# Kernel optimization log

Measured on AMD Instinct MI355X. Metric: run time of the kernel, lower is better.

## Reference

```python
import jax, jax.numpy as jnp
import numpy as np

N_STEPS = 20      # max(n_steps_al, n_steps_kc)
ALPHA   = 0.9     # membrane decay exp(-dt/tau_m)
V_TH    = 1.0     # spiking threshold
G_SOMA  = 0.3     # dendrite->axon coupling conductance (2-compartment KC)
APL_GAIN = 1.0    # graded APL gain
I_SCALE = 0.5     # graded ORN drive scale
BETA    = 10.0    # surrogate-gradient sharpness ('soft' sigmoid)

@jax.custom_vjp
def spike(x):
    return (x > 0).astype(x.dtype)

def _spike_fwd(x):
    return spike(x), x

def _spike_bwd(x, g):
    s = jax.nn.sigmoid(BETA * x)
    return (g * BETA * s * (1.0 - s),)

spike.defvjp(_spike_fwd, _spike_bwd)


def _sparse_w(key, shape, density):
    k1, k2 = jax.random.split(key)
    mask = jax.random.bernoulli(k1, density, shape)
    w = jax.random.uniform(k2, shape)
    return (mask * w).astype(jnp.float32)


def setup_inputs() -> dict:
    key = jax.random.key(0)
    ks = jax.random.split(key, 10)
    batch, n_or, n_orn, n_ln, n_pn, n_kc, n_odors = 4096, 21, 42, 56, 42, 2000, 34
    or_input = jax.random.uniform(ks[0], (batch, n_or), dtype=jnp.float32)
    or_gains = jnp.ones((n_or,), jnp.float32)
    # fixed OR->ORN mapping: OR i drives left (2i) and right (2i+1) ORNs
    m = np.zeros((n_or, n_orn), np.float32)
    for i in range(n_or):
        m[i, 2 * i] = 1.0
        m[i, 2 * i + 1] = 1.0
    mapping = jnp.asarray(m)
    orn_to_pn = _sparse_w(ks[1], (n_orn, n_pn), 0.3)
    orn_to_ln = _sparse_w(ks[2], (n_orn, n_ln), 0.3)
    ln_to_pn = _sparse_w(ks[3], (n_ln, n_pn), 0.3)
    pn_to_kc = _sparse_w(ks[4], (n_pn, n_kc), 0.15)  # ~6 PN claws per KC
    kc_to_apl = jax.random.uniform(ks[5], (n_kc, 1), dtype=jnp.float32) * 0.01
    apl_to_kc = jax.random.uniform(ks[6], (1, n_kc), dtype=jnp.float32)
    dec_w = jax.random.normal(ks[7], (n_kc, n_odors), dtype=jnp.float32) * 0.02
    dec_b = jnp.zeros((n_odors,), jnp.float32)
    return {"or_input": or_input, "or_gains": or_gains, "mapping": mapping,
            "orn_to_pn": orn_to_pn, "orn_to_ln": orn_to_ln, "ln_to_pn": ln_to_pn,
            "pn_to_kc": pn_to_kc, "kc_to_apl": kc_to_apl, "apl_to_kc": apl_to_kc,
            "dec_w": dec_w, "dec_b": dec_b}


def reference(or_input, or_gains, mapping, orn_to_pn, orn_to_ln, ln_to_pn,
              pn_to_kc, kc_to_apl, apl_to_kc, dec_w, dec_b):
    B = or_input.shape[0]
    n_orn, n_pn = orn_to_pn.shape
    n_ln = orn_to_ln.shape[1]
    n_kc = pn_to_kc.shape[1]
    # OR transduction: graded, learnable per-OR gain
    orn_drive = (or_input * jax.nn.softplus(or_gains)) @ mapping  # [B, n_orn]

    z = lambda n: jnp.zeros((B, n), or_input.dtype)
    carry0 = (z(n_orn), z(n_ln), z(n_pn), z(n_kc), z(n_kc), z(1), z(n_kc))

    def step(carry, _):
        v_orn, v_ln, v_pn, v_d, v_a, apl, kc_cnt = carry
        # ORN LIF driven by graded OR current
        v_orn = ALPHA * v_orn + I_SCALE * orn_drive
        s_orn = spike(v_orn - V_TH)
        v_orn = v_orn * (1.0 - s_orn)
        # LN LIF (lateral inhibition interneurons)
        v_ln = ALPHA * v_ln + s_orn @ orn_to_ln
        s_ln = spike(v_ln - V_TH)
        v_ln = v_ln * (1.0 - s_ln)
        # PN LIF: ORN excitation, LN inhibition
        v_pn = ALPHA * v_pn + s_orn @ orn_to_pn - s_ln @ ln_to_pn
        s_pn = spike(v_pn - V_TH)
        v_pn = v_pn * (1.0 - s_pn)
        # KC 2-compartment: dendrite gets PN input and APL inhibition
        v_d = ALPHA * v_d + s_pn @ pn_to_kc - apl @ apl_to_kc
        v_a = ALPHA * v_a + G_SOMA * (v_d - v_a)
        s_kc = spike(v_a - V_TH)
        v_a = v_a * (1.0 - s_kc)
        # APL: graded (non-spiking) global inhibition from KC spikes
        apl = APL_GAIN * jax.nn.relu(s_kc @ kc_to_apl)
        return (v_orn, v_ln, v_pn, v_d, v_a, apl, kc_cnt + s_kc), None

    carry, _ = jax.lax.scan(step, carry0, None, length=N_STEPS)
    kc_count = carry[-1]
    kc_rates = kc_count / N_STEPS
    logits = kc_rates @ dec_w + dec_b  # [B, n_odors]
    return logits
```

## Files before the change

### kernel.cpp

```cpp
#include <hip/hip_runtime.h>

#define NSTEPS 20
#define ALPHA  0.9f
#define VTH    1.0f
#define GSOMA  0.3f
#define ISCALE 0.5f

#define NOR  21
#define NORN 42
#define NLN  56
#define NPN  42
#define NKC  2000
#define NOD  34

#define TPB  256
#define KPER 8

typedef float v2f __attribute__((ext_vector_type(2)));
typedef float v4f __attribute__((ext_vector_type(4)));

#define PK_ADD(d, a) asm("v_pk_add_f32 %0, %1, %0" : "+v"(d) : "v"(a))
#define PK_FMA(d, b, f) asm("v_pk_fma_f32 %0, %1, %2, %0" : "+v"(d) : "v"(b), "v"(f))

__global__ __launch_bounds__(64)
void phase1a(const float* __restrict__ or_input,
             const float* __restrict__ or_gains,
             const float* __restrict__ mapping,
             const float* __restrict__ orn_to_ln,
             ulonglong2* __restrict__ gAB,
             int batch)
{
    const int lane = threadIdx.x;
    const int row  = blockIdx.x;
    if (row >= batch) return;

    const int jl = lane < NLN ? lane : 0;
    float wOl[NORN];
#pragma unroll
    for (int o = 0; o < NORN; ++o) wOl[o] = orn_to_ln[o * NLN + jl];

    float spg = 0.f;
    if (lane < NOR) spg = log1pf(expf(or_gains[lane]));

    float drive = 0.f;
    {
        const float* x = or_input + (long)row * NOR;
        const int jo = lane < NORN ? lane : 0;
#pragma unroll
        for (int i = 0; i < NOR; ++i) {
            float g = __shfl(spg, i);
            drive += x[i] * g * mapping[i * NORN + jo];
        }
        drive *= ISCALE;
    }

    float v_orn = 0.f, v_ln = 0.f;
    ulonglong2* outm = gAB + (long)row * NSTEPS;

    for (int t = 0; t < NSTEPS; ++t) {
        bool so = false;
        if (lane < NORN) {
            v_orn = ALPHA * v_orn + drive;
            so = (v_orn - VTH) > 0.f;
            if (so) v_orn = 0.f;
        }
        const unsigned long long mOrn = __ballot(so);
        const unsigned int mo_lo = (unsigned int)mOrn;
        const unsigned int mo_hi = (unsigned int)(mOrn >> 32);

        float aln = 0.f;
#pragma unroll
        for (int o = 0; o < 32; ++o) aln += (float)((mo_lo >> o) & 1u) * wOl[o];
#pragma unroll
        for (int o = 32; o < NORN; ++o) aln += (float)((mo_hi >> (o - 32)) & 1u) * wOl[o];

        bool sl = false;
        if (lane < NLN) {
            v_ln = ALPHA * v_ln + aln;
            sl = (v_ln - VTH) > 0.f;
            if (sl) v_ln = 0.f;
        }
        const unsigned long long mLn = __ballot(sl);
        if (lane == 0) outm[t] = make_ulonglong2(mOrn, mLn);
    }
}

__global__ __launch_bounds__(64)
void phase1b(const float* __restrict__ orn_to_pn,
             const float* __restrict__ ln_to_pn,
             const ulonglong2* __restrict__ gAB,
             unsigned long long* __restrict__ gPN,
             int batch)
{
    const int lane = threadIdx.x;
    const int row  = blockIdx.x;
    if (row >= batch) return;

    const int jp = lane < NPN ? lane : 0;
    float wOp[NORN], wLp[NLN];
#pragma unroll
    for (int o = 0; o < NORN; ++o) wOp[o] = orn_to_pn[o * NPN + jp];
#pragma unroll
    for (int l = 0; l < NLN; ++l) wLp[l] = ln_to_pn[l * NPN + jp];

    const ulonglong2* inm = gAB + (long)row * NSTEPS;
    unsigned long long* outm = gPN + (long)row * NSTEPS;

    float v_pn = 0.f;
    ulonglong2 ab = inm[0];

    for (int t = 0; t < NSTEPS; ++t) {
        ulonglong2 abn;
        if (t < NSTEPS - 1) abn = inm[t + 1];

        const unsigned int mo_lo = (unsigned int)ab.x;
        const unsigned int mo_hi = (unsigned int)(ab.x >> 32);
        const unsigned int ml_lo = (unsigned int)ab.y;
        const unsigned int ml_hi = (unsigned int)(ab.y >> 32);

        float apn = 0.f;
#pragma unroll
        for (int o = 0; o < 32; ++o) apn += (float)((mo_lo >> o) & 1u) * wOp[o];
#pragma unroll
        for (int o = 32; o < NORN; ++o) apn += (float)((mo_hi >> (o - 32)) & 1u) * wOp[o];

        float h = 0.f;
#pragma unroll
        for (int l = 0; l < 32; ++l) h += (float)((ml_lo >> l) & 1u) * wLp[l];
#pragma unroll
        for (int l = 32; l < NLN; ++l) h += (float)((ml_hi >> (l - 32)) & 1u) * wLp[l];

        bool sp = false;
        if (lane < NPN) {
            v_pn = ALPHA * v_pn + apn - h;
            sp = (v_pn - VTH) > 0.f;
            if (sp) v_pn = 0.f;
        }
        const unsigned long long mPn = __ballot(sp);
        if (lane == 0) outm[t] = mPn;
        ab = abn;
    }
}

__global__ __launch_bounds__(TPB)
void phase2_pkc(const unsigned long long* __restrict__ g_masks,
                const float* __restrict__ pn_to_kc,
                const float* __restrict__ kc_to_apl,
                const float* __restrict__ apl_to_kc,
                const float* __restrict__ dec_w,
                const float* __restrict__ dec_b,
                float* __restrict__ out)
{
    __shared__ float sRed[2][4];
    __shared__ float sRed2[4 * NOD];

    const int tid  = threadIdx.x;
    const int lane = tid & 63;
    const int wid  = tid >> 6;
    const int b    = blockIdx.x;

    const int  kbase = tid * KPER;
    const bool act   = (kbase < NKC);
    v2f   vd2[4];
    float va[KPER], cnt[KPER], wa2k[KPER], wk2a[KPER];
#pragma unroll
    for (int k = 0; k < 4; ++k) vd2[k] = (v2f)(0.f);
#pragma unroll
    for (int j = 0; j < KPER; ++j) { va[j] = 0.f; cnt[j] = 0.f; }
    {
        const int idx = act ? kbase : 0;
        const float4* a4 = (const float4*)(apl_to_kc + idx);
        const float4* k4 = (const float4*)(kc_to_apl + idx);
        float4 a0 = a4[0], a1 = a4[1], k0 = k4[0], k1 = k4[1];
        const float g = act ? 1.f : 0.f;
        wa2k[0] = g * a0.x; wa2k[1] = g * a0.y; wa2k[2] = g * a0.z; wa2k[3] = g * a0.w;
        wa2k[4] = g * a1.x; wa2k[5] = g * a1.y; wa2k[6] = g * a1.z; wa2k[7] = g * a1.w;
        wk2a[0] = g * k0.x; wk2a[1] = g * k0.y; wk2a[2] = g * k0.z; wk2a[3] = g * k0.w;
        wk2a[4] = g * k1.x; wk2a[5] = g * k1.y; wk2a[6] = g * k1.z; wk2a[7] = g * k1.w;
    }
    if (tid < 8) sRed[tid >> 2][tid & 3] = 0.f;
    __syncthreads();

    const unsigned long long* gm = g_masks + (long)b * NSTEPS;
    unsigned long long mcur = gm[0];

    for (int t = 0; t < NSTEPS; ++t) {
        unsigned long long mnext;
        if (t < NSTEPS - 1) mnext = gm[t + 1];

        const float* rp = sRed[(t + 1) & 1];
        const float apl = fmaxf(rp[0] + rp[1] + rp[2] + rp[3], 0.f);

#pragma unroll
        for (int j = 0; j < KPER; ++j)
            vd2[j >> 1][j & 1] = ALPHA * vd2[j >> 1][j & 1] - apl * wa2k[j];

        unsigned long long m = mcur;
        while (m) {
            const int p0 = __builtin_ctzll(m); m &= m - 1;
            int p1 = p0; float f1 = 0.f;
            if (m) { p1 = __builtin_ctzll(m); m &= m - 1; f1 = 1.f; }
            if (act) {
                const v4f* w0 = (const v4f*)(pn_to_kc + (long)p0 * NKC + kbase);
                const v4f* w1 = (const v4f*)(pn_to_kc + (long)p1 * NKC + kbase);
                v4f A0 = w0[0], A1 = w0[1];
                v4f B0 = w1[0], B1 = w1[1];
                v2f f2; f2[0] = f1; f2[1] = f1;
                PK_ADD(vd2[0], A0.xy); PK_ADD(vd2[1], A0.zw);
                PK_ADD(vd2[2], A1.xy); PK_ADD(vd2[3], A1.zw);
                PK_FMA(vd2[0], B0.xy, f2); PK_FMA(vd2[1], B0.zw, f2);
                PK_FMA(vd2[2], B1.xy, f2); PK_FMA(vd2[3], B1.zw, f2);
            }
        }

        float aplp = 0.f;
#pragma unroll
        for (int j = 0; j < KPER; ++j) {
            va[j] = ALPHA * va[j] + GSOMA * (vd2[j >> 1][j & 1] - va[j]);
            const bool c = (va[j] - VTH) > 0.f;
            const float s = c ? 1.f : 0.f;
            va[j] = c ? 0.f : va[j];
            cnt[j] += s;
            aplp += s * wk2a[j];
        }
        for (int off = 32; off > 0; off >>= 1) aplp += __shfl_xor(aplp, off, 64);
        if (lane == 0) sRed[t & 1][wid] = aplp;
        __syncthreads();
        mcur = mnext;
    }

    float acc[NOD];
#pragma unroll
    for (int o = 0; o < NOD; ++o) acc[o] = 0.f;
    if (act) {
#pragma unroll
        for (int j = 0; j < KPER; ++j) {
            float r = cnt[j] / 20.0f;
            if (r != 0.f) {
                const float* wr = dec_w + (long)(kbase + j) * NOD;
#pragma unroll
                for (int o = 0; o < NOD; ++o) acc[o] += r * wr[o];
            }
        }
    }
#pragma unroll
    for (int o = 0; o < NOD; ++o) {
        float v = acc[o];
        for (int off = 32; off > 0; off >>= 1) v += __shfl_xor(v, off, 64);
        if (lane == 0) sRed2[wid * NOD + o] = v;
    }
    __syncthreads();
    if (tid < NOD) {
        float v = sRed2[tid] + sRed2[NOD + tid] + sRed2[2 * NOD + tid] +
                  sRed2[3 * NOD + tid] + dec_b[tid];
        out[(long)b * NOD + tid] = v;
    }
}

__global__ __launch_bounds__(TPB)
void snn_fused(const float* __restrict__ or_input, const float* __restrict__ or_gains,
               const float* __restrict__ mapping, const float* __restrict__ orn_to_pn,
               const float* __restrict__ orn_to_ln, const float* __restrict__ ln_to_pn,
               const float* __restrict__ pn_to_kc, const float* __restrict__ kc_to_apl,
               const float* __restrict__ apl_to_kc, const float* __restrict__ dec_w,
               const float* __restrict__ dec_b, float* __restrict__ out)
{
    __shared__ float sW_ol[NORN * NLN];
    __shared__ float sW_op[NORN * NPN];
    __shared__ float sW_lp[NLN * NPN];
    __shared__ float sDrive[NORN];
    __shared__ float sSpg[NOR];
    __shared__ float sOrn[NORN];
    __shared__ float sLn[NLN];
    __shared__ float sApl;
    __shared__ float sRed[4];
    __shared__ float sRed2[4 * NOD];
    __shared__ unsigned long long sMask;

    const int tid = threadIdx.x;
    const int b   = blockIdx.x;

    for (int i = tid; i < NORN * NLN; i += TPB) sW_ol[i] = orn_to_ln[i];
    for (int i = tid; i < NORN * NPN; i += TPB) sW_op[i] = orn_to_pn[i];
    for (int i = tid; i < NLN * NPN;  i += TPB) sW_lp[i] = ln_to_pn[i];
    if (tid < NOR) sSpg[tid] = log1pf(expf(or_gains[tid]));
    if (tid == 0)  sApl = 0.f;
    __syncthreads();

    if (tid < NORN) {
        const float* x = or_input + (long)b * NOR;
        float d = 0.f;
        for (int i = 0; i < NOR; ++i) d += x[i] * sSpg[i] * mapping[i * NORN + tid];
        sDrive[tid] = d * ISCALE;
    }

    const int  kbase = tid * KPER;
    const bool act   = (kbase < NKC);
    float vd[KPER], va[KPER], cnt[KPER], wa2k[KPER], wk2a[KPER];
#pragma unroll
    for (int j = 0; j < KPER; ++j) {
        vd[j] = 0.f; va[j] = 0.f; cnt[j] = 0.f;
        wa2k[j] = act ? apl_to_kc[kbase + j] : 0.f;
        wk2a[j] = act ? kc_to_apl[kbase + j] : 0.f;
    }
    float v_orn = 0.f, v_ln = 0.f, v_pn = 0.f, v_pn_exc = 0.f;
    __syncthreads();

    for (int t = 0; t < NSTEPS; ++t) {
        if (tid < NORN) {
            v_orn = ALPHA * v_orn + sDrive[tid];
            float s = (v_orn - VTH) > 0.f ? 1.f : 0.f;
            v_orn *= (1.f - s);
            sOrn[tid] = s;
        }
        __syncthreads();
        if (tid < NLN) {
            float a = 0.f;
            for (int o = 0; o < NORN; ++o) a += sOrn[o] * sW_ol[o * NLN + tid];
            v_ln = ALPHA * v_ln + a;
            float s = (v_ln - VTH) > 0.f ? 1.f : 0.f;
            v_ln *= (1.f - s);
            sLn[tid] = s;
        } else if (tid >= 64 && tid < 64 + NPN) {
            const int j = tid - 64;
            float a = 0.f;
            for (int o = 0; o < NORN; ++o) a += sOrn[o] * sW_op[o * NPN + j];
            v_pn_exc = a;
        }
        __syncthreads();
        if (tid >= 64 && tid < 64 + NPN) {
            const int j = tid - 64;
            float inh = 0.f;
            for (int l = 0; l < NLN; ++l) inh += sLn[l] * sW_lp[l * NPN + j];
            v_pn = ALPHA * v_pn + v_pn_exc - inh;
            bool s = (v_pn - VTH) > 0.f;
            if (s) v_pn = 0.f;
            unsigned long long bal = __ballot(s);
            if (tid == 64) sMask = bal;
        }
        __syncthreads();
        {
            const float apl = sApl;
#pragma unroll
            for (int j = 0; j < KPER; ++j) vd[j] = ALPHA * vd[j] - apl * wa2k[j];
            unsigned long long m = sMask;
            while (m) {
                const int p = __builtin_ctzll(m);
                m &= m - 1;
                if (act) {
                    const float4* w = (const float4*)(pn_to_kc + (long)p * NKC + kbase);
                    float4 w0 = w[0], w1 = w[1];
                    vd[0] += w0.x; vd[1] += w0.y; vd[2] += w0.z; vd[3] += w0.w;
                    vd[4] += w1.x; vd[5] += w1.y; vd[6] += w1.z; vd[7] += w1.w;
                }
            }
            float aplp = 0.f;
#pragma unroll
            for (int j = 0; j < KPER; ++j) {
                va[j] = ALPHA * va[j] + GSOMA * (vd[j] - va[j]);
                float s = (va[j] - VTH) > 0.f ? 1.f : 0.f;
                va[j] *= (1.f - s);
                cnt[j] += s;
                aplp += s * wk2a[j];
            }
            for (int off = 32; off > 0; off >>= 1) aplp += __shfl_xor(aplp, off, 64);
            if ((tid & 63) == 0) sRed[tid >> 6] = aplp;
        }
        __syncthreads();
        if (tid == 0) {
            float a = sRed[0] + sRed[1] + sRed[2] + sRed[3];
            sApl = fmaxf(a, 0.f);
        }
    }

    float acc[NOD];
#pragma unroll
    for (int o = 0; o < NOD; ++o) acc[o] = 0.f;
    if (act) {
#pragma unroll
        for (int j = 0; j < KPER; ++j) {
            float r = cnt[j] / 20.0f;
            if (r != 0.f) {
                const float* wr = dec_w + (long)(kbase + j) * NOD;
#pragma unroll
                for (int o = 0; o < NOD; ++o) acc[o] += r * wr[o];
            }
        }
    }
#pragma unroll
    for (int o = 0; o < NOD; ++o) {
        float v = acc[o];
        for (int off = 32; off > 0; off >>= 1) v += __shfl_xor(v, off, 64);
        if ((tid & 63) == 0) sRed2[(tid >> 6) * NOD + o] = v;
    }
    __syncthreads();
    if (tid < NOD) {
        float v = sRed2[tid] + sRed2[NOD + tid] + sRed2[2 * NOD + tid] +
                  sRed2[3 * NOD + tid] + dec_b[tid];
        out[(long)b * NOD + tid] = v;
    }
}

extern "C" void kernel_launch(void* const* d_in, const int* in_sizes, int n_in,
                              void* d_out, int out_size, void* d_ws, size_t ws_size,
                              hipStream_t stream) {
    (void)n_in; (void)out_size;
    const float* or_input  = (const float*)d_in[0];
    const float* or_gains  = (const float*)d_in[1];
    const float* mapping   = (const float*)d_in[2];
    const float* orn_to_pn = (const float*)d_in[3];
    const float* orn_to_ln = (const float*)d_in[4];
    const float* ln_to_pn  = (const float*)d_in[5];
    const float* pn_to_kc  = (const float*)d_in[6];
    const float* kc_to_apl = (const float*)d_in[7];
    const float* apl_to_kc = (const float*)d_in[8];
    const float* dec_w     = (const float*)d_in[9];
    const float* dec_b     = (const float*)d_in[10];
    float* out = (float*)d_out;

    const int batch = in_sizes[0] / NOR;
    const size_t needAB = (size_t)batch * NSTEPS * sizeof(ulonglong2);
    const size_t needPN = (size_t)batch * NSTEPS * sizeof(unsigned long long);

    if (ws_size >= needAB + needPN) {
        ulonglong2* gAB = (ulonglong2*)d_ws;
        unsigned long long* gPN = (unsigned long long*)((char*)d_ws + needAB);
        hipLaunchKernelGGL(phase1a, dim3(batch), dim3(64), 0, stream,
                           or_input, or_gains, mapping, orn_to_ln, gAB, batch);
        hipLaunchKernelGGL(phase1b, dim3(batch), dim3(64), 0, stream,
                           orn_to_pn, ln_to_pn, gAB, gPN, batch);
        hipLaunchKernelGGL(phase2_pkc, dim3(batch), dim3(TPB), 0, stream,
                           gPN, pn_to_kc, kc_to_apl, apl_to_kc, dec_w, dec_b, out);
    } else {
        hipLaunchKernelGGL(snn_fused, dim3(batch), dim3(TPB), 0, stream,
                           or_input, or_gains, mapping, orn_to_pn, orn_to_ln,
                           ln_to_pn, pn_to_kc, kc_to_apl, apl_to_kc, dec_w, dec_b, out);
    }
}
```

Measured before the change: 215.9 us.

## Run KC phase with a single wavefront per batch row to remove block barriers

```diff
diff --git a/kernel.cpp b/kernel.cpp
--- a/kernel.cpp
+++ b/kernel.cpp
@@ -15,12 +15,7 @@
 
 #define TPB  256
 #define KPER 8
-
-typedef float v2f __attribute__((ext_vector_type(2)));
-typedef float v4f __attribute__((ext_vector_type(4)));
-
-#define PK_ADD(d, a) asm("v_pk_add_f32 %0, %1, %0" : "+v"(d) : "v"(a))
-#define PK_FMA(d, b, f) asm("v_pk_fma_f32 %0, %1, %2, %0" : "+v"(d) : "v"(b), "v"(f))
+#define KPW  32
 
 __global__ __launch_bounds__(64)
 void phase1a(const float* __restrict__ or_input,
@@ -142,118 +137,136 @@
     }
 }
 
-__global__ __launch_bounds__(TPB)
-void phase2_pkc(const unsigned long long* __restrict__ g_masks,
-                const float* __restrict__ pn_to_kc,
-                const float* __restrict__ kc_to_apl,
-                const float* __restrict__ apl_to_kc,
-                const float* __restrict__ dec_w,
-                const float* __restrict__ dec_b,
-                float* __restrict__ out)
+__global__ __launch_bounds__(64)
+void phase2_w1(const unsigned long long* __restrict__ g_masks,
+               const float* __restrict__ pn_to_kc,
+               const float* __restrict__ kc_to_apl,
+               const float* __restrict__ apl_to_kc,
+               const float* __restrict__ dec_w,
+               const float* __restrict__ dec_b,
+               float* __restrict__ out)
 {
-    __shared__ float sRed[2][4];
-    __shared__ float sRed2[4 * NOD];
-
-    const int tid  = threadIdx.x;
-    const int lane = tid & 63;
-    const int wid  = tid >> 6;
-    const int b    = blockIdx.x;
-
-    const int  kbase = tid * KPER;
-    const bool act   = (kbase < NKC);
-    v2f   vd2[4];
-    float va[KPER], cnt[KPER], wa2k[KPER], wk2a[KPER];
-#pragma unroll
-    for (int k = 0; k < 4; ++k) vd2[k] = (v2f)(0.f);
-#pragma unroll
-    for (int j = 0; j < KPER; ++j) { va[j] = 0.f; cnt[j] = 0.f; }
-    {
-        const int idx = act ? kbase : 0;
-        const float4* a4 = (const float4*)(apl_to_kc + idx);
-        const float4* k4 = (const float4*)(kc_to_apl + idx);
-        float4 a0 = a4[0], a1 = a4[1], k0 = k4[0], k1 = k4[1];
-        const float g = act ? 1.f : 0.f;
-        wa2k[0] = g * a0.x; wa2k[1] = g * a0.y; wa2k[2] = g * a0.z; wa2k[3] = g * a0.w;
-        wa2k[4] = g * a1.x; wa2k[5] = g * a1.y; wa2k[6] = g * a1.z; wa2k[7] = g * a1.w;
-        wk2a[0] = g * k0.x; wk2a[1] = g * k0.y; wk2a[2] = g * k0.z; wk2a[3] = g * k0.w;
-        wk2a[4] = g * k1.x; wk2a[5] = g * k1.y; wk2a[6] = g * k1.z; wk2a[7] = g * k1.w;
-    }
-    if (tid < 8) sRed[tid >> 2][tid & 3] = 0.f;
-    __syncthreads();
+    const int lane  = threadIdx.x;
+    const int b     = blockIdx.x;
+    const int kbase = lane * KPW;
+
+    bool vk[4];
+#pragma unroll
+    for (int k = 0; k < 4; ++k) vk[k] = (kbase + k * 8) < NKC;
+
+    float vd[KPW], va[KPW], cnt[KPW], wa2k[KPW], wk2a[KPW];
+#pragma unroll
+    for (int j = 0; j < KPW; ++j) { vd[j] = 0.f; va[j] = 0.f; cnt[j] = 0.f; }
+
+#pragma unroll
+    for (int q = 0; q < 8; ++q) {
+        const int k   = q >> 1;
+        const int idx = vk[k] ? (kbase + q * 4) : 0;
+        const float g = vk[k] ? 1.f : 0.f;
+        float4 a = *(const float4*)(apl_to_kc + idx);
+        float4 c = *(const float4*)(kc_to_apl + idx);
+        wa2k[q * 4 + 0] = g * a.x; wa2k[q * 4 + 1] = g * a.y;
+        wa2k[q * 4 + 2] = g * a.z; wa2k[q * 4 + 3] = g * a.w;
+        wk2a[q * 4 + 0] = g * c.x; wk2a[q * 4 + 1] = g * c.y;
+        wk2a[q * 4 + 2] = g * c.z; wk2a[q * 4 + 3] = g * c.w;
+    }
 
     const unsigned long long* gm = g_masks + (long)b * NSTEPS;
     unsigned long long mcur = gm[0];
+    float apl = 0.f;
 
     for (int t = 0; t < NSTEPS; ++t) {
         unsigned long long mnext;
         if (t < NSTEPS - 1) mnext = gm[t + 1];
 
-        const float* rp = sRed[(t + 1) & 1];
-        const float apl = fmaxf(rp[0] + rp[1] + rp[2] + rp[3], 0.f);
-
-#pragma unroll
-        for (int j = 0; j < KPER; ++j)
-            vd2[j >> 1][j & 1] = ALPHA * vd2[j >> 1][j & 1] - apl * wa2k[j];
+#pragma unroll
+        for (int j = 0; j < KPW; ++j) vd[j] = ALPHA * vd[j] - apl * wa2k[j];
 
         unsigned long long m = mcur;
         while (m) {
             const int p0 = __builtin_ctzll(m); m &= m - 1;
             int p1 = p0; float f1 = 0.f;
             if (m) { p1 = __builtin_ctzll(m); m &= m - 1; f1 = 1.f; }
-            if (act) {
-                const v4f* w0 = (const v4f*)(pn_to_kc + (long)p0 * NKC + kbase);
-                const v4f* w1 = (const v4f*)(pn_to_kc + (long)p1 * NKC + kbase);
-                v4f A0 = w0[0], A1 = w0[1];
-                v4f B0 = w1[0], B1 = w1[1];
-                v2f f2; f2[0] = f1; f2[1] = f1;
-                PK_ADD(vd2[0], A0.xy); PK_ADD(vd2[1], A0.zw);
-                PK_ADD(vd2[2], A1.xy); PK_ADD(vd2[3], A1.zw);
-                PK_FMA(vd2[0], B0.xy, f2); PK_FMA(vd2[1], B0.zw, f2);
-                PK_FMA(vd2[2], B1.xy, f2); PK_FMA(vd2[3], B1.zw, f2);
+            const float* r0 = pn_to_kc + (long)p0 * NKC;
+            const float* r1 = pn_to_kc + (long)p1 * NKC;
+#pragma unroll
+            for (int k = 0; k < 4; ++k) {
+                const int off = vk[k] ? (kbase + k * 8) : 0;
+                float4 A0 = *(const float4*)(r0 + off);
+                float4 A1 = *(const float4*)(r0 + off + 4);
+                float4 B0 = *(const float4*)(r1 + off);
+                float4 B1 = *(const float4*)(r1 + off + 4);
+                vd[k*8+0] += A0.x; vd[k*8+1] += A0.y; vd[k*8+2] += A0.z; vd[k*8+3] += A0.w;
+                vd[k*8+4] += A1.x; vd[k*8+5] += A1.y; vd[k*8+6] += A1.z; vd[k*8+7] += A1.w;
+                vd[k*8+0] += f1 * B0.x; vd[k*8+1] += f1 * B0.y;
+                vd[k*8+2] += f1 * B0.z; vd[k*8+3] += f1 * B0.w;
+                vd[k*8+4] += f1 * B1.x; vd[k*8+5] += f1 * B1.y;
+                vd[k*8+6] += f1 * B1.z; vd[k*8+7] += f1 * B1.w;
             }
         }
 
-        float aplp = 0.f;
-#pragma unroll
-        for (int j = 0; j < KPER; ++j) {
-            va[j] = ALPHA * va[j] + GSOMA * (vd2[j >> 1][j & 1] - va[j]);
+        float p[4] = {0.f, 0.f, 0.f, 0.f};
+#pragma unroll
+        for (int j = 0; j < KPW; ++j) {
+            va[j] = ALPHA * va[j] + GSOMA * (vd[j] - va[j]);
             const bool c = (va[j] - VTH) > 0.f;
             const float s = c ? 1.f : 0.f;
             va[j] = c ? 0.f : va[j];
             cnt[j] += s;
-            aplp += s * wk2a[j];
-        }
-        for (int off = 32; off > 0; off >>= 1) aplp += __shfl_xor(aplp, off, 64);
-        if (lane == 0) sRed[t & 1][wid] = aplp;
-        __syncthreads();
+            p[j >> 3] += s * wk2a[j];
+        }
+
+#pragma unroll
+        for (int k = 0; k < 4; ++k) p[k] += __shfl_xor(p[k], 8, 64);
+#pragma unroll
+        for (int k = 0; k < 4; ++k) p[k] += __shfl_xor(p[k], 4, 64);
+#pragma unroll
+        for (int k = 0; k < 4; ++k) p[k] += __shfl_xor(p[k], 2, 64);
+#pragma unroll
+        for (int k = 0; k < 4; ++k) p[k] += __shfl_xor(p[k], 1, 64);
+        const float u0 = p[0] + p[2];
+        const float u1 = p[1] + p[3];
+        const float W  = u0 + u1;
+        const float s0 = __shfl(W, 0, 64);
+        const float s1 = __shfl(W, 16, 64);
+        const float s2 = __shfl(W, 32, 64);
+        const float s3 = __shfl(W, 48, 64);
+        apl = fmaxf(((s0 + s1) + s2) + s3, 0.f);
+
         mcur = mnext;
     }
 
-    float acc[NOD];
-#pragma unroll
-    for (int o = 0; o < NOD; ++o) acc[o] = 0.f;
-    if (act) {
-#pragma unroll
-        for (int j = 0; j < KPER; ++j) {
-            float r = cnt[j] / 20.0f;
-            if (r != 0.f) {
-                const float* wr = dec_w + (long)(kbase + j) * NOD;
-#pragma unroll
-                for (int o = 0; o < NOD; ++o) acc[o] += r * wr[o];
-            }
-        }
-    }
-#pragma unroll
+    unsigned int rmask = 0u;
+#pragma unroll
+    for (int j = 0; j < KPW; ++j) {
+        cnt[j] = cnt[j] / 20.0f;
+        if (vk[j >> 3] && cnt[j] != 0.f) rmask |= (1u << j);
+    }
+
     for (int o = 0; o < NOD; ++o) {
-        float v = acc[o];
-        for (int off = 32; off > 0; off >>= 1) v += __shfl_xor(v, off, 64);
-        if (lane == 0) sRed2[wid * NOD + o] = v;
-    }
-    __syncthreads();
-    if (tid < NOD) {
-        float v = sRed2[tid] + sRed2[NOD + tid] + sRed2[2 * NOD + tid] +
-                  sRed2[3 * NOD + tid] + dec_b[tid];
-        out[(long)b * NOD + tid] = v;
+        float p[4] = {0.f, 0.f, 0.f, 0.f};
+        unsigned int mm = rmask;
+        while (mm) {
+            const int j = (int)__builtin_ctz(mm); mm &= mm - 1;
+            p[j >> 3] += cnt[j] * dec_w[(long)(kbase + j) * NOD + o];
+        }
+#pragma unroll
+        for (int k = 0; k < 4; ++k) p[k] += __shfl_xor(p[k], 8, 64);
+#pragma unroll
+        for (int k = 0; k < 4; ++k) p[k] += __shfl_xor(p[k], 4, 64);
+#pragma unroll
+        for (int k = 0; k < 4; ++k) p[k] += __shfl_xor(p[k], 2, 64);
+#pragma unroll
+        for (int k = 0; k < 4; ++k) p[k] += __shfl_xor(p[k], 1, 64);
+        const float u0 = p[0] + p[2];
+        const float u1 = p[1] + p[3];
+        const float W  = u0 + u1;
+        const float s0 = __shfl(W, 0, 64);
+        const float s1 = __shfl(W, 16, 64);
+        const float s2 = __shfl(W, 32, 64);
+        const float s3 = __shfl(W, 48, 64);
+        const float tot = ((s0 + s1) + s2) + s3 + dec_b[o];
+        if (lane == 0) out[(long)b * NOD + o] = tot;
     }
 }
 
@@ -429,7 +442,7 @@
                            or_input, or_gains, mapping, orn_to_ln, gAB, batch);
         hipLaunchKernelGGL(phase1b, dim3(batch), dim3(64), 0, stream,
                            orn_to_pn, ln_to_pn, gAB, gPN, batch);
-        hipLaunchKernelGGL(phase2_pkc, dim3(batch), dim3(TPB), 0, stream,
+        hipLaunchKernelGGL(phase2_w1, dim3(batch), dim3(64), 0, stream,
                            gPN, pn_to_kc, kc_to_apl, apl_to_kc, dec_w, dec_b, out);
     } else {
         hipLaunchKernelGGL(snn_fused, dim3(batch), dim3(TPB), 0, stream,
```

Result: slower. 250.6 us (+16.1%).
